# Performance work log

Measured on AMD Instinct MI355X. Metric: run time of the kernel, lower is better.

The kernel has to match this reference:

```python
import jax, jax.numpy as jnp
import numpy as np

N, B, CIN = 2048, 16, 1
M = 4096
COUT = 64
R = 128


def setup_inputs() -> dict:
    key = jax.random.key(0)
    k1, k2, k3, k4, k5 = jax.random.split(key, 5)
    return {
        "context_in": jax.random.normal(k1, (N, B, CIN), dtype=jnp.float32),
        "context_out": jax.random.normal(k2, (N, B, COUT), dtype=jnp.float32),
        "target_in": jax.random.normal(k3, (M, B, CIN), dtype=jnp.float32),
        "lengthscale": jnp.ones((1,), dtype=jnp.float32),
        "W": jax.random.normal(k4, (R, COUT + 1), dtype=jnp.float32),
        "b": jax.random.normal(k5, (R,), dtype=jnp.float32),
    }


def reference(context_in, context_out, target_in, lengthscale, W, b):
    # context_in: (N,B,Cin), context_out: (N,B,Cout), target_in: (M,B,Cin)
    n, batch, _ = context_in.shape
    # density channel prepended -> (N,B,Cout+1)
    dens = jnp.ones((n, batch, 1), dtype=context_in.dtype)
    co = jnp.concatenate([dens, context_out], axis=-1)
    ci = jnp.transpose(context_in, (1, 0, 2))   # (B,N,Cin)
    ti = jnp.transpose(target_in, (1, 0, 2))    # (B,M,Cin)
    # squared pairwise distances (B,N,M)
    d2 = (jnp.sum(ci * ci, -1)[:, :, None]
          + jnp.sum(ti * ti, -1)[:, None, :]
          - 2.0 * jnp.einsum('bnd,bmd->bnm', ci, ti))
    d2 = jnp.maximum(d2, 0.0)
    # RBF kernel: exp(-0.5 * d2 / lengthscale^2)
    K = jnp.exp(-0.5 * d2 / (lengthscale[0] ** 2))  # (B,N,M)
    # weighted sum over context points: (B,M,Cout+1)
    out = jnp.einsum('nbc,bnm->bmc', co, K)
    # density normalization of non-density channels
    out = jnp.concatenate([out[..., :1], out[..., 1:] / (out[..., :1] + 1e-8)], axis=-1)
    # linear projection (Cout+1 -> R)
    out = out @ W.T + b
    return jnp.transpose(out, (1, 0, 2))  # (M,B,R)
```

## Files before the change

kernel.cpp:

```cpp
#include <hip/hip_runtime.h>
#include <hip/hip_bf16.h>


#define N_CTX 2048
#define BATCH 16
#define M_TGT 4096
#define COUT  64
#define RDIM  128

#define WS_CO_BYTES (N_CTX * BATCH * COUT * 2)
#define WS_SXA_OFF  WS_CO_BYTES
#define WS_SXB_OFF  (WS_SXA_OFF + N_CTX * BATCH * 4)
#define WS_WT_OFF   (WS_SXB_OFF + N_CTX * BATCH * 4)

#define SSCALE 0.8493222f

typedef __attribute__((ext_vector_type(8)))  short        bf16x8;
typedef __attribute__((ext_vector_type(4)))  float        floatx4;
typedef __attribute__((ext_vector_type(4)))  unsigned int uint4v;

#if __has_builtin(__builtin_amdgcn_exp2f)
#define EXP2F __builtin_amdgcn_exp2f
#else
#define EXP2F exp2f
#endif

static __device__ __forceinline__ unsigned int pack_bf16(float lo, float hi) {
    __hip_bfloat162 h = __float22bfloat162_rn(make_float2(lo, hi));
    return *reinterpret_cast<unsigned int*>(&h);
}
static __device__ __forceinline__ unsigned short f2bf(float f) {
    __hip_bfloat16 h = __float2bfloat16(f);
    return *reinterpret_cast<unsigned short*>(&h);
}

__global__ __launch_bounds__(256)
void convdeepset_prep(const float* __restrict__ ci, const float* __restrict__ co,
                      const float* __restrict__ ls, const float* __restrict__ W,
                      unsigned char* __restrict__ ws)
{
    unsigned short* cow = (unsigned short*)ws;
    float*          sxa = (float*)(ws + WS_SXA_OFF);
    float*          sxb = (float*)(ws + WS_SXB_OFF);
    unsigned short* wt  = (unsigned short*)(ws + WS_WT_OFF);
    const int blk = blockIdx.x, tid = threadIdx.x;

    if (blk < 1024) {
        const int g    = blk * 4 + (tid >> 6);
        const int bb   = g & 15;
        const int nblk = g >> 4;
        const int c    = tid & 63;
        const float* rp = co + ((size_t)nblk * 8 * BATCH + bb) * COUT + c;
        unsigned int u[4];
#pragma unroll
        for (int j = 0; j < 4; ++j) {
            const float f0 = rp[(size_t)(2 * j)     * BATCH * COUT];
            const float f1 = rp[(size_t)(2 * j + 1) * BATCH * COUT];
            u[j] = pack_bf16(f0, f1);
        }
        *(uint4v*)&cow[(size_t)bb * 131072 + nblk * 512 + c * 8] = *(uint4v*)u;
    } else if (blk < 1152) {
        const int f = (blk - 1024) * 256 + tid;
        const int n = f & 2047, bb = f >> 11;
        const float s = SSCALE / ls[0];
        const float v = s * ci[(size_t)n * BATCH + bb];
        sxa[bb * 2048 + n] = v + v;
        sxb[bb * 2048 + n] = -v * v;
    } else {
        for (int f = tid; f < 8192; f += 256) {
            const int cp = f & 7, r = (f >> 3) & 127, ch = f >> 10;
            wt[ch * 1024 + r * 8 + cp] = f2bf(W[r * 65 + 1 + ch * 8 + cp]);
        }
    }
}

struct Slot {
    bf16x8  c0, c1, c2, c3;
    floatx4 xa0, xa1, xb0, xb1;
};

__global__ __launch_bounds__(256, 2)
void convdeepset_main(const float* __restrict__ ti, const float* __restrict__ ls,
                      const float* __restrict__ W,  const float* __restrict__ bias,
                      const unsigned char* __restrict__ ws, float* __restrict__ out)
{
    __shared__ float sxal[N_CTX];
    __shared__ float sxbl[N_CTX];
    __shared__ float xred[4][64][20];
    __shared__ unsigned short vstage[4][2][1024];

    const int tid  = threadIdx.x;
    const int lane = tid & 63;
    const int wv   = tid >> 6;
    const int g2   = lane >> 4;
    const int l15  = lane & 15;
    const int wpr  = wv >> 1;
    const int half = wv & 1;

    const int xcd = blockIdx.x & 7;
    const int i   = blockIdx.x >> 3;
    const int b   = xcd * 2 + (i & 1);
    const int mt  = i >> 1;
    const int m0  = mt * 128 + wpr * 64;

    const float4* sag = (const float4*)(ws + WS_SXA_OFF) + b * (N_CTX / 4);
    const float4* sbg = (const float4*)(ws + WS_SXB_OFF) + b * (N_CTX / 4);
    ((float4*)sxal)[tid]       = sag[tid];
    ((float4*)sxal)[tid + 256] = sag[tid + 256];
    ((float4*)sxbl)[tid]       = sbg[tid];
    ((float4*)sxbl)[tid + 256] = sbg[tid + 256];

    const float s = SSCALE / ls[0];
    float syv[4];
#pragma unroll
    for (int t = 0; t < 4; ++t)
        syv[t] = s * ti[(size_t)(m0 + t * 16 + l15) * BATCH + b];

    const unsigned short* cowb = (const unsigned short*)ws
                               + (size_t)b * 131072 + (size_t)half * 65536;
    const int xoff = half * 1024;

    const short onebf = (short)0x3F80;
    bf16x8 ones;
#pragma unroll
    for (int j = 0; j < 8; ++j) ones[j] = onebf;

    floatx4 acc[4][4], accd[4];
#pragma unroll
    for (int t = 0; t < 4; ++t) {
#pragma unroll
        for (int q = 0; q < 4; ++q)
#pragma unroll
            for (int e = 0; e < 4; ++e) acc[t][q][e] = 0.0f;
#pragma unroll
        for (int e = 0; e < 4; ++e) accd[t][e] = 0.0f;
    }

    auto loadk = [&](Slot& S, int k) {
        const unsigned short* bp = cowb + ((k * 4 + g2) << 9) + l15 * 8;
        S.c0 = *(const bf16x8*)(bp);
        S.c1 = *(const bf16x8*)(bp + 128);
        S.c2 = *(const bf16x8*)(bp + 256);
        S.c3 = *(const bf16x8*)(bp + 384);
        const float* ap  = &sxal[xoff + k * 32 + g2 * 8];
        const float* bpx = &sxbl[xoff + k * 32 + g2 * 8];
        S.xa0 = *(const floatx4*)(ap);
        S.xa1 = *(const floatx4*)(ap + 4);
        S.xb0 = *(const floatx4*)(bpx);
        S.xb1 = *(const floatx4*)(bpx + 4);
    };

    auto compute = [&](const Slot& S) {
#pragma unroll
        for (int t = 0; t < 4; ++t) {
            const float sy = syv[t];
            const floatx4 a0 = S.xa0 * sy + S.xb0;
            const floatx4 a1 = S.xa1 * sy + S.xb1;
            float kv[8];
            kv[0] = EXP2F(a0.x); kv[1] = EXP2F(a0.y);
            kv[2] = EXP2F(a0.z); kv[3] = EXP2F(a0.w);
            kv[4] = EXP2F(a1.x); kv[5] = EXP2F(a1.y);
            kv[6] = EXP2F(a1.z); kv[7] = EXP2F(a1.w);
            uint4v aw;
#pragma unroll
            for (int q = 0; q < 4; ++q)
                aw[q] = pack_bf16(kv[2 * q], kv[2 * q + 1]);
            const bf16x8 av = __builtin_bit_cast(bf16x8, aw);
            acc[t][0] = __builtin_amdgcn_mfma_f32_16x16x32_bf16(av, S.c0, acc[t][0], 0, 0, 0);
            acc[t][1] = __builtin_amdgcn_mfma_f32_16x16x32_bf16(av, S.c1, acc[t][1], 0, 0, 0);
            acc[t][2] = __builtin_amdgcn_mfma_f32_16x16x32_bf16(av, S.c2, acc[t][2], 0, 0, 0);
            acc[t][3] = __builtin_amdgcn_mfma_f32_16x16x32_bf16(av, S.c3, acc[t][3], 0, 0, 0);
            accd[t]   = __builtin_amdgcn_mfma_f32_16x16x32_bf16(av, ones, accd[t], 0, 0, 0);
        }
    };

    __syncthreads();
    Slot A, B;
    loadk(A, 0);
    for (int p = 0; p < 32; p += 2) {
        loadk(B, p + 1);
        compute(A);
        if (p + 2 < 32) loadk(A, p + 2);
        compute(B);
    }

#pragma unroll
    for (int j = 0; j < 2; ++j) {
        float* xw = &xred[wv][lane][0];
        if (half == 0) {
            *(floatx4*)&xw[0]  = acc[2 + j][0];
            *(floatx4*)&xw[4]  = acc[2 + j][1];
            *(floatx4*)&xw[8]  = acc[2 + j][2];
            *(floatx4*)&xw[12] = acc[2 + j][3];
            *(floatx4*)&xw[16] = accd[2 + j];
        } else {
            *(floatx4*)&xw[0]  = acc[j][0];
            *(floatx4*)&xw[4]  = acc[j][1];
            *(floatx4*)&xw[8]  = acc[j][2];
            *(floatx4*)&xw[12] = acc[j][3];
            *(floatx4*)&xw[16] = accd[j];
        }
        __syncthreads();
        const float* xr = &xred[wv ^ 1][lane][0];
        if (half == 0) {
            acc[j][0] += *(const floatx4*)&xr[0];
            acc[j][1] += *(const floatx4*)&xr[4];
            acc[j][2] += *(const floatx4*)&xr[8];
            acc[j][3] += *(const floatx4*)&xr[12];
            accd[j]   += *(const floatx4*)&xr[16];
        } else {
            acc[2 + j][0] += *(const floatx4*)&xr[0];
            acc[2 + j][1] += *(const floatx4*)&xr[4];
            acc[2 + j][2] += *(const floatx4*)&xr[8];
            acc[2 + j][3] += *(const floatx4*)&xr[12];
            accd[2 + j]   += *(const floatx4*)&xr[16];
        }
        __syncthreads();
    }

    const unsigned short* wtg = (const unsigned short*)(ws + WS_WT_OFF);

    auto epi = [&](const floatx4 (&a)[4], const floatx4 ad, float syt, int t, int tt) {
        const float sysq = syt * syt;
        const int   mrow = m0 + t * 16;
        float dt[4], ff[4];
#pragma unroll
        for (int reg = 0; reg < 4; ++reg) {
            const int m   = (lane >> 4) * 4 + reg;
            const float ysq = __shfl(sysq, m, 64);
            const float e   = EXP2F(-ysq);
            dt[reg] = ad[reg] * e;
            ff[reg] = e / (dt[reg] + 1e-8f);
        }
        unsigned short* vs = vstage[wv][tt];
#pragma unroll
        for (int reg = 0; reg < 4; ++reg) {
            const int m = (lane >> 4) * 4 + reg;
#pragma unroll
            for (int q = 0; q < 4; ++q) {
                const int c = q * 16 + l15;
                vs[(c >> 3) * 128 + m * 8 + (c & 7)] = f2bf(a[q][reg]);
            }
        }
        floatx4 pacc[8];
#pragma unroll
        for (int rt = 0; rt < 8; ++rt)
#pragma unroll
            for (int e = 0; e < 4; ++e) pacc[rt][e] = 0.0f;
#pragma unroll
        for (int s2 = 0; s2 < 2; ++s2) {
            const int ch = s2 * 4 + g2;
            const bf16x8 avp = *(const bf16x8*)&vs[ch * 128 + l15 * 8];
#pragma unroll
            for (int rt = 0; rt < 8; ++rt) {
                const bf16x8 bvp = *(const bf16x8*)&wtg[ch * 1024 + (rt * 16 + l15) * 8];
                pacc[rt] = __builtin_amdgcn_mfma_f32_16x16x32_bf16(avp, bvp, pacc[rt], 0, 0, 0);
            }
        }
#pragma unroll
        for (int rt = 0; rt < 8; ++rt) {
            const int r = rt * 16 + l15;
            const float w0v = W[r * 65];
            const float bv  = bias[r];
#pragma unroll
            for (int reg = 0; reg < 4; ++reg) {
                const int m = (lane >> 4) * 4 + reg;
                out[((size_t)(mrow + m) * BATCH + b) * RDIM + r]
                    = pacc[rt][reg] * ff[reg] + dt[reg] * w0v + bv;
            }
        }
    };

    if (half == 0) {
        epi(acc[0], accd[0], syv[0], 0, 0);
        epi(acc[1], accd[1], syv[1], 1, 1);
    } else {
        epi(acc[2], accd[2], syv[2], 2, 0);
        epi(acc[3], accd[3], syv[3], 3, 1);
    }
}

extern "C" void kernel_launch(void* const* d_in, const int* in_sizes, int n_in,
                              void* d_out, int out_size, void* d_ws, size_t ws_size,
                              hipStream_t stream) {
    const float* ci   = (const float*)d_in[0];
    const float* co   = (const float*)d_in[1];
    const float* ti   = (const float*)d_in[2];
    const float* ls   = (const float*)d_in[3];
    const float* W    = (const float*)d_in[4];
    const float* bias = (const float*)d_in[5];
    float* o = (float*)d_out;
    (void)in_sizes; (void)n_in; (void)out_size; (void)ws_size;

    convdeepset_prep<<<1153, 256, 0, stream>>>(ci, co, ls, W, (unsigned char*)d_ws);
    convdeepset_main<<<512, 256, 0, stream>>>(
        ti, ls, W, bias, (const unsigned char*)d_ws, o);
}
```

Measured before the change: 116.8 us.

## Split context dimension across four waves with 64-target tiles and two-stage reduction

Each block now covers 64 targets instead of 128, and each of the four waves handles a quarter of the context points. The partial sums are combined through a two-stage shared-memory reduction, and the grid doubles to 1024 blocks with launch bounds raised to four blocks per CU. The second context term is now recomputed from the first (-v*v = -(2v)^2/4) rather than loaded, which drops one shared array. The explicit double-buffered register prefetch is removed to lower register pressure, so the kernel now depends on occupancy rather than software pipelining to hide load latency.

```diff
diff --git a/kernel.cpp b/kernel.cpp
--- a/kernel.cpp
+++ b/kernel.cpp
@@ -32,6 +32,14 @@
 static __device__ __forceinline__ unsigned short f2bf(float f) {
     __hip_bfloat16 h = __float2bfloat16(f);
     return *reinterpret_cast<unsigned short*>(&h);
+}
+static __device__ __forceinline__ floatx4 fma4(floatx4 a, float s, floatx4 b) {
+    floatx4 r;
+    r.x = __builtin_fmaf(a.x, s, b.x);
+    r.y = __builtin_fmaf(a.y, s, b.y);
+    r.z = __builtin_fmaf(a.z, s, b.z);
+    r.w = __builtin_fmaf(a.w, s, b.w);
+    return r;
 }
 
 __global__ __launch_bounds__(256)
@@ -74,41 +82,31 @@
     }
 }
 
-struct Slot {
-    bf16x8  c0, c1, c2, c3;
-    floatx4 xa0, xa1, xb0, xb1;
-};
-
-__global__ __launch_bounds__(256, 2)
+__global__ __launch_bounds__(256, 4)
 void convdeepset_main(const float* __restrict__ ti, const float* __restrict__ ls,
                       const float* __restrict__ W,  const float* __restrict__ bias,
                       const unsigned char* __restrict__ ws, float* __restrict__ out)
 {
     __shared__ float sxal[N_CTX];
-    __shared__ float sxbl[N_CTX];
     __shared__ float xred[4][64][20];
-    __shared__ unsigned short vstage[4][2][1024];
+    __shared__ unsigned short vstage[4][1024];
 
     const int tid  = threadIdx.x;
     const int lane = tid & 63;
     const int wv   = tid >> 6;
     const int g2   = lane >> 4;
     const int l15  = lane & 15;
-    const int wpr  = wv >> 1;
-    const int half = wv & 1;
+    const int q01  = wv & 1;
 
     const int xcd = blockIdx.x & 7;
     const int i   = blockIdx.x >> 3;
     const int b   = xcd * 2 + (i & 1);
     const int mt  = i >> 1;
-    const int m0  = mt * 128 + wpr * 64;
+    const int m0  = mt * 64;
 
     const float4* sag = (const float4*)(ws + WS_SXA_OFF) + b * (N_CTX / 4);
-    const float4* sbg = (const float4*)(ws + WS_SXB_OFF) + b * (N_CTX / 4);
     ((float4*)sxal)[tid]       = sag[tid];
     ((float4*)sxal)[tid + 256] = sag[tid + 256];
-    ((float4*)sxbl)[tid]       = sbg[tid];
-    ((float4*)sxbl)[tid + 256] = sbg[tid + 256];
 
     const float s = SSCALE / ls[0];
     float syv[4];
@@ -116,9 +114,10 @@
     for (int t = 0; t < 4; ++t)
         syv[t] = s * ti[(size_t)(m0 + t * 16 + l15) * BATCH + b];
 
-    const unsigned short* cowb = (const unsigned short*)ws
-                               + (size_t)b * 131072 + (size_t)half * 65536;
-    const int xoff = half * 1024;
+    const unsigned short* bp = (const unsigned short*)ws
+                             + (size_t)b * 131072 + (size_t)wv * 32768
+                             + (g2 << 9) + l15 * 8;
+    const float* xap = &sxal[wv * 512 + g2 * 8];
 
     const short onebf = (short)0x3F80;
     bf16x8 ones;
@@ -136,26 +135,24 @@
         for (int e = 0; e < 4; ++e) accd[t][e] = 0.0f;
     }
 
-    auto loadk = [&](Slot& S, int k) {
-        const unsigned short* bp = cowb + ((k * 4 + g2) << 9) + l15 * 8;
-        S.c0 = *(const bf16x8*)(bp);
-        S.c1 = *(const bf16x8*)(bp + 128);
-        S.c2 = *(const bf16x8*)(bp + 256);
-        S.c3 = *(const bf16x8*)(bp + 384);
-        const float* ap  = &sxal[xoff + k * 32 + g2 * 8];
-        const float* bpx = &sxbl[xoff + k * 32 + g2 * 8];
-        S.xa0 = *(const floatx4*)(ap);
-        S.xa1 = *(const floatx4*)(ap + 4);
-        S.xb0 = *(const floatx4*)(bpx);
-        S.xb1 = *(const floatx4*)(bpx + 4);
-    };
-
-    auto compute = [&](const Slot& S) {
+    __syncthreads();
+
+    for (int k = 0; k < 16; ++k) {
+        const bf16x8 c0 = *(const bf16x8*)(bp);
+        const bf16x8 c1 = *(const bf16x8*)(bp + 128);
+        const bf16x8 c2 = *(const bf16x8*)(bp + 256);
+        const bf16x8 c3 = *(const bf16x8*)(bp + 384);
+        bp += 2048;
+        const floatx4 xa0 = *(const floatx4*)(xap);
+        const floatx4 xa1 = *(const floatx4*)(xap + 4);
+        xap += 32;
+        const floatx4 xb0 = xa0 * (xa0 * -0.25f);
+        const floatx4 xb1 = xa1 * (xa1 * -0.25f);
 #pragma unroll
         for (int t = 0; t < 4; ++t) {
             const float sy = syv[t];
-            const floatx4 a0 = S.xa0 * sy + S.xb0;
-            const floatx4 a1 = S.xa1 * sy + S.xb1;
+            const floatx4 a0 = fma4(xa0, sy, xb0);
+            const floatx4 a1 = fma4(xa1, sy, xb1);
             float kv[8];
             kv[0] = EXP2F(a0.x); kv[1] = EXP2F(a0.y);
             kv[2] = EXP2F(a0.z); kv[3] = EXP2F(a0.w);
@@ -166,28 +163,18 @@
             for (int q = 0; q < 4; ++q)
                 aw[q] = pack_bf16(kv[2 * q], kv[2 * q + 1]);
             const bf16x8 av = __builtin_bit_cast(bf16x8, aw);
-            acc[t][0] = __builtin_amdgcn_mfma_f32_16x16x32_bf16(av, S.c0, acc[t][0], 0, 0, 0);
-            acc[t][1] = __builtin_amdgcn_mfma_f32_16x16x32_bf16(av, S.c1, acc[t][1], 0, 0, 0);
-            acc[t][2] = __builtin_amdgcn_mfma_f32_16x16x32_bf16(av, S.c2, acc[t][2], 0, 0, 0);
-            acc[t][3] = __builtin_amdgcn_mfma_f32_16x16x32_bf16(av, S.c3, acc[t][3], 0, 0, 0);
+            acc[t][0] = __builtin_amdgcn_mfma_f32_16x16x32_bf16(av, c0, acc[t][0], 0, 0, 0);
+            acc[t][1] = __builtin_amdgcn_mfma_f32_16x16x32_bf16(av, c1, acc[t][1], 0, 0, 0);
+            acc[t][2] = __builtin_amdgcn_mfma_f32_16x16x32_bf16(av, c2, acc[t][2], 0, 0, 0);
+            acc[t][3] = __builtin_amdgcn_mfma_f32_16x16x32_bf16(av, c3, acc[t][3], 0, 0, 0);
             accd[t]   = __builtin_amdgcn_mfma_f32_16x16x32_bf16(av, ones, accd[t], 0, 0, 0);
         }
-    };
-
-    __syncthreads();
-    Slot A, B;
-    loadk(A, 0);
-    for (int p = 0; p < 32; p += 2) {
-        loadk(B, p + 1);
-        compute(A);
-        if (p + 2 < 32) loadk(A, p + 2);
-        compute(B);
     }
 
 #pragma unroll
     for (int j = 0; j < 2; ++j) {
         float* xw = &xred[wv][lane][0];
-        if (half == 0) {
+        if (q01 == 0) {
             *(floatx4*)&xw[0]  = acc[2 + j][0];
             *(floatx4*)&xw[4]  = acc[2 + j][1];
             *(floatx4*)&xw[8]  = acc[2 + j][2];
@@ -202,7 +189,7 @@
         }
         __syncthreads();
         const float* xr = &xred[wv ^ 1][lane][0];
-        if (half == 0) {
+        if (q01 == 0) {
             acc[j][0] += *(const floatx4*)&xr[0];
             acc[j][1] += *(const floatx4*)&xr[4];
             acc[j][2] += *(const floatx4*)&xr[8];
@@ -218,9 +205,25 @@
         __syncthreads();
     }
 
+    {
+        float* xw = &xred[wv][lane][0];
+        const int st = (wv == 0) ? 1 : (wv == 1) ? 3 : (wv == 2) ? 0 : 2;
+        if (st == 0)      { *(floatx4*)&xw[0] = acc[0][0]; *(floatx4*)&xw[4] = acc[0][1]; *(floatx4*)&xw[8] = acc[0][2]; *(floatx4*)&xw[12] = acc[0][3]; *(floatx4*)&xw[16] = accd[0]; }
+        else if (st == 1) { *(floatx4*)&xw[0] = acc[1][0]; *(floatx4*)&xw[4] = acc[1][1]; *(floatx4*)&xw[8] = acc[1][2]; *(floatx4*)&xw[12] = acc[1][3]; *(floatx4*)&xw[16] = accd[1]; }
+        else if (st == 2) { *(floatx4*)&xw[0] = acc[2][0]; *(floatx4*)&xw[4] = acc[2][1]; *(floatx4*)&xw[8] = acc[2][2]; *(floatx4*)&xw[12] = acc[2][3]; *(floatx4*)&xw[16] = accd[2]; }
+        else              { *(floatx4*)&xw[0] = acc[3][0]; *(floatx4*)&xw[4] = acc[3][1]; *(floatx4*)&xw[8] = acc[3][2]; *(floatx4*)&xw[12] = acc[3][3]; *(floatx4*)&xw[16] = accd[3]; }
+        __syncthreads();
+        const float* xr = &xred[wv ^ 2][lane][0];
+        const int rt = (wv == 0) ? 0 : (wv == 1) ? 2 : (wv == 2) ? 1 : 3;
+        if (rt == 0)      { acc[0][0] += *(const floatx4*)&xr[0]; acc[0][1] += *(const floatx4*)&xr[4]; acc[0][2] += *(const floatx4*)&xr[8]; acc[0][3] += *(const floatx4*)&xr[12]; accd[0] += *(const floatx4*)&xr[16]; }
+        else if (rt == 1) { acc[1][0] += *(const floatx4*)&xr[0]; acc[1][1] += *(const floatx4*)&xr[4]; acc[1][2] += *(const floatx4*)&xr[8]; acc[1][3] += *(const floatx4*)&xr[12]; accd[1] += *(const floatx4*)&xr[16]; }
+        else if (rt == 2) { acc[2][0] += *(const floatx4*)&xr[0]; acc[2][1] += *(const floatx4*)&xr[4]; acc[2][2] += *(const floatx4*)&xr[8]; acc[2][3] += *(const floatx4*)&xr[12]; accd[2] += *(const floatx4*)&xr[16]; }
+        else              { acc[3][0] += *(const floatx4*)&xr[0]; acc[3][1] += *(const floatx4*)&xr[4]; acc[3][2] += *(const floatx4*)&xr[8]; acc[3][3] += *(const floatx4*)&xr[12]; accd[3] += *(const floatx4*)&xr[16]; }
+    }
+
     const unsigned short* wtg = (const unsigned short*)(ws + WS_WT_OFF);
 
-    auto epi = [&](const floatx4 (&a)[4], const floatx4 ad, float syt, int t, int tt) {
+    auto epi = [&](const floatx4 (&a)[4], const floatx4 ad, float syt, int t) {
         const float sysq = syt * syt;
         const int   mrow = m0 + t * 16;
         float dt[4], ff[4];
@@ -232,7 +235,7 @@
             dt[reg] = ad[reg] * e;
             ff[reg] = e / (dt[reg] + 1e-8f);
         }
-        unsigned short* vs = vstage[wv][tt];
+        unsigned short* vs = vstage[wv];
 #pragma unroll
         for (int reg = 0; reg < 4; ++reg) {
             const int m = (lane >> 4) * 4 + reg;
@@ -244,40 +247,37 @@
         }
         floatx4 pacc[8];
 #pragma unroll
-        for (int rt = 0; rt < 8; ++rt)
-#pragma unroll
-            for (int e = 0; e < 4; ++e) pacc[rt][e] = 0.0f;
+        for (int r8 = 0; r8 < 8; ++r8)
+#pragma unroll
+            for (int e = 0; e < 4; ++e) pacc[r8][e] = 0.0f;
 #pragma unroll
         for (int s2 = 0; s2 < 2; ++s2) {
             const int ch = s2 * 4 + g2;
             const bf16x8 avp = *(const bf16x8*)&vs[ch * 128 + l15 * 8];
 #pragma unroll
-            for (int rt = 0; rt < 8; ++rt) {
-                const bf16x8 bvp = *(const bf16x8*)&wtg[ch * 1024 + (rt * 16 + l15) * 8];
-                pacc[rt] = __builtin_amdgcn_mfma_f32_16x16x32_bf16(avp, bvp, pacc[rt], 0, 0, 0);
+            for (int r8 = 0; r8 < 8; ++r8) {
+                const bf16x8 bvp = *(const bf16x8*)&wtg[ch * 1024 + (r8 * 16 + l15) * 8];
+                pacc[r8] = __builtin_amdgcn_mfma_f32_16x16x32_bf16(avp, bvp, pacc[r8], 0, 0, 0);
             }
         }
 #pragma unroll
-        for (int rt = 0; rt < 8; ++rt) {
-            const int r = rt * 16 + l15;
+        for (int r8 = 0; r8 < 8; ++r8) {
+            const int r = r8 * 16 + l15;
             const float w0v = W[r * 65];
             const float bv  = bias[r];
 #pragma unroll
             for (int reg = 0; reg < 4; ++reg) {
                 const int m = (lane >> 4) * 4 + reg;
                 out[((size_t)(mrow + m) * BATCH + b) * RDIM + r]
-                    = pacc[rt][reg] * ff[reg] + dt[reg] * w0v + bv;
+                    = pacc[r8][reg] * ff[reg] + dt[reg] * w0v + bv;
             }
         }
     };
 
-    if (half == 0) {
-        epi(acc[0], accd[0], syv[0], 0, 0);
-        epi(acc[1], accd[1], syv[1], 1, 1);
-    } else {
-        epi(acc[2], accd[2], syv[2], 2, 0);
-        epi(acc[3], accd[3], syv[3], 3, 1);
-    }
+    if (wv == 0)      epi(acc[0], accd[0], syv[0], 0);
+    else if (wv == 1) epi(acc[2], accd[2], syv[2], 2);
+    else if (wv == 2) epi(acc[1], accd[1], syv[1], 1);
+    else              epi(acc[3], accd[3], syv[3], 3);
 }
 
 extern "C" void kernel_launch(void* const* d_in, const int* in_sizes, int n_in,
@@ -293,6 +293,6 @@
     (void)in_sizes; (void)n_in; (void)out_size; (void)ws_size;
 
     convdeepset_prep<<<1153, 256, 0, stream>>>(ci, co, ls, W, (unsigned char*)d_ws);
-    convdeepset_main<<<512, 256, 0, stream>>>(
+    convdeepset_main<<<1024, 256, 0, stream>>>(
         ti, ls, W, bias, (const unsigned char*)d_ws, o);
 }
```

After: 128.3 us. 1.1x slower.
